# Kernel optimization log

Hardware: AMD Instinct MI355X
Metric: run time of the kernel (lower is better)

Reference implementation:

```python
import jax, jax.numpy as jnp
import numpy as np
import math

B, L, H, E = 4, 1024, 8, 64  # win_size = L
NEG_INF = -1e9  # finite stand-in for -inf causal mask (same softmax result, grad-safe)


def setup_inputs() -> dict:
    key = jax.random.key(0)
    k1, k2, k3, k4 = jax.random.split(key, 4)
    return {
        "queries": jax.random.normal(k1, (B, L, H, E), dtype=jnp.float32),
        "keys": jax.random.normal(k2, (B, L, H, E), dtype=jnp.float32),
        "values": jax.random.normal(k3, (B, L, H, E), dtype=jnp.float32),
        "sigma": jax.random.normal(k4, (B, L, H), dtype=jnp.float32),
    }


def reference(queries, keys, values, sigma):
    b, l, h, e = queries.shape
    scale = 1.0 / math.sqrt(e)

    # attention scores: [B,H,L,S]
    scores = jnp.einsum('blhe,bshe->bhls', queries, keys)
    causal = jnp.triu(jnp.ones((l, l), dtype=bool), k=1)  # mask_flag=True, attn_mask=None
    scores = jnp.where(causal, NEG_INF, scores)
    attn = scale * scores

    # sigma chain: [B,L,H] -> [B,H,L] -> [B,H,L,L]
    s = jnp.transpose(sigma, (0, 2, 1))
    s = jax.nn.sigmoid(s * 5.0) + 1e-5
    s = jnp.power(3.0, s) - 1.0
    sigma4 = jnp.broadcast_to(s[..., None], (b, h, l, l))

    # gaussian prior over |i-j| distances
    idx = jnp.arange(l)
    dist = jnp.abs(idx[:, None] - idx[None, :]).astype(attn.dtype)  # [L,L]
    prior = jnp.exp(-(dist ** 2) / (2.0 * sigma4 ** 2)) / (math.sqrt(2.0 * math.pi) * sigma4)

    series = jax.nn.softmax(attn, axis=-1)  # dropout is identity at eval
    V = jnp.einsum('bhls,bshd->blhd', series, values)
    return V, series, prior, sigma4
```

## Files before the change

kernel.cpp:

```cpp
#include <hip/hip_runtime.h>
#include <math.h>
#include <stdint.h>


#define BB 4
#define LL 1024
#define HH 8
#define EE 64
#define ROWS 32
#define THREADS 1024
#define CHUNK 128

typedef __attribute__((ext_vector_type(8))) short bf16x8;
typedef __attribute__((ext_vector_type(4))) float f32x4;

static constexpr size_t OFF_V      = 0;
static constexpr size_t OFF_SERIES = (size_t)BB * LL * HH * EE;
static constexpr size_t OFF_PRIOR  = OFF_SERIES + (size_t)BB * HH * LL * LL;
static constexpr size_t OFF_SIGMA4 = OFF_PRIOR + (size_t)BB * HH * LL * LL;

static constexpr int LDS_BYTES = 82048;

__device__ __forceinline__ short f2bf(float f) {
    union { float f; uint32_t u; } v; v.f = f;
    uint32_t r = (v.u + 0x7FFFu + ((v.u >> 16) & 1u)) >> 16;
    return (short)r;
}
__device__ __forceinline__ float bf2f(short s) {
    union { uint32_t u; float f; } v; v.u = ((uint32_t)(unsigned short)s) << 16;
    return v.f;
}

__global__ __launch_bounds__(THREADS, 4) void anomaly_attn_kernel(
    const float* __restrict__ Q, const float* __restrict__ K,
    const float* __restrict__ V, float* __restrict__ out)
{
    extern __shared__ char lds[];
    short* sSb  = (short*)lds;
    short* Kb   = (short*)(lds + 65536);
    float* red  = (float*)(lds + 65536);
    float* rinv = (float*)(lds + 81920);

    const int tid  = threadIdx.x;
    const int lane = tid & 63;
    const int w    = tid >> 6;
    const int tile = blockIdx.x & 31;
    const int bh   = blockIdx.x >> 5;
    const int b    = bh >> 3, h = bh & 7;
    const int r0   = tile * ROWS;
    const int NCH  = (r0 + ROWS + CHUNK - 1) / CHUNK;
    const int NC   = NCH * CHUNK;

    const float* Kbase = K + (size_t)b * (LL * HH * EE) + h * EE;
    const float* Vbase = V + (size_t)b * (LL * HH * EE) + h * EE;

    const int jr2 = tid >> 3;
    const int g8  = tid & 7;

    const int rgQ = w >> 3;
    const int cgQ = w & 7;
    bf16x8 qf0, qf1;
    {
        int qrow = r0 + rgQ * 16 + (lane & 15);
        const float* qp = Q + ((size_t)(b * LL + qrow) * HH + h) * EE + ((lane >> 4) << 3);
        float4 a = *(const float4*)qp;
        float4 c = *(const float4*)(qp + 4);
        qf0[0]=f2bf(a.x); qf0[1]=f2bf(a.y); qf0[2]=f2bf(a.z); qf0[3]=f2bf(a.w);
        qf0[4]=f2bf(c.x); qf0[5]=f2bf(c.y); qf0[6]=f2bf(c.z); qf0[7]=f2bf(c.w);
        float4 a2 = *(const float4*)(qp + 32);
        float4 c2 = *(const float4*)(qp + 36);
        qf1[0]=f2bf(a2.x); qf1[1]=f2bf(a2.y); qf1[2]=f2bf(a2.z); qf1[3]=f2bf(a2.w);
        qf1[4]=f2bf(c2.x); qf1[5]=f2bf(c2.y); qf1[6]=f2bf(c2.z); qf1[7]=f2bf(c2.w);
    }

    float4 kp0 = *(const float4*)&Kbase[(size_t)jr2 * 512 + g8 * 8];
    float4 kp1 = *(const float4*)&Kbase[(size_t)jr2 * 512 + g8 * 8 + 4];

    for (int ck = 0; ck < NCH; ++ck) {
        __syncthreads();
        {
            bf16x8 kv;
            kv[0]=f2bf(kp0.x); kv[1]=f2bf(kp0.y); kv[2]=f2bf(kp0.z); kv[3]=f2bf(kp0.w);
            kv[4]=f2bf(kp1.x); kv[5]=f2bf(kp1.y); kv[6]=f2bf(kp1.z); kv[7]=f2bf(kp1.w);
            *(bf16x8*)&Kb[jr2 * 64 + ((g8 ^ (jr2 & 7)) << 3)] = kv;
        }
        if (ck + 1 < NCH) {
            kp0 = *(const float4*)&Kbase[(size_t)((ck + 1) * CHUNK + jr2) * 512 + g8 * 8];
            kp1 = *(const float4*)&Kbase[(size_t)((ck + 1) * CHUNK + jr2) * 512 + g8 * 8 + 4];
        }
        __syncthreads();

        f32x4 acc = {0.f, 0.f, 0.f, 0.f};
        const int jl = cgQ * 16 + (lane & 15);
        {
            int ge = lane >> 4;
            bf16x8 bf = *(const bf16x8*)&Kb[jl * 64 + ((ge ^ (jl & 7)) << 3)];
            acc = __builtin_amdgcn_mfma_f32_16x16x32_bf16(qf0, bf, acc, 0, 0, 0);
            ge = 4 + (lane >> 4);
            bf16x8 bf2 = *(const bf16x8*)&Kb[jl * 64 + ((ge ^ (jl & 7)) << 3)];
            acc = __builtin_amdgcn_mfma_f32_16x16x32_bf16(qf1, bf2, acc, 0, 0, 0);
        }
        int colg = ck * CHUNK + cgQ * 16 + (lane & 15);
        int gc   = colg >> 3;
        int co   = colg & 7;
#pragma unroll
        for (int q = 0; q < 4; ++q) {
            int rt = rgQ * 16 + ((lane >> 4) << 2) + q;
            float e = (colg <= r0 + rt) ? __expf(acc[q] * 0.125f) : 0.f;
            sSb[rt * 1024 + ((gc ^ (rt & 7)) << 3) + co] = f2bf(e);
        }
    }
    __syncthreads();

    float4 vp0 = *(const float4*)&Vbase[(size_t)jr2 * 512 + g8 * 8];
    float4 vp1 = *(const float4*)&Vbase[(size_t)jr2 * 512 + g8 * 8 + 4];

    {
        int r = tid >> 5, j2 = tid & 31;
        float sum = 0.f;
        for (int g = j2; g < (NC >> 3); g += 32) {
            bf16x8 v = *(const bf16x8*)&sSb[r * 1024 + ((g ^ (r & 7)) << 3)];
            float s0 = bf2f(v[0]) + bf2f(v[1]), s1 = bf2f(v[2]) + bf2f(v[3]);
            float s2 = bf2f(v[4]) + bf2f(v[5]), s3 = bf2f(v[6]) + bf2f(v[7]);
            sum += (s0 + s1) + (s2 + s3);
        }
        sum += __shfl_xor(sum, 1);
        sum += __shfl_xor(sum, 2);
        sum += __shfl_xor(sum, 4);
        sum += __shfl_xor(sum, 8);
        sum += __shfl_xor(sum, 16);
        if (j2 == 0) rinv[r] = 1.0f / sum;
    }
    __syncthreads();

    {
        int gc = tid & 127;
        int rb = tid >> 7;
        size_t base = OFF_SERIES + ((size_t)bh * LL + r0) * LL;
#pragma unroll
        for (int it = 0; it < 4; ++it) {
            int r_ = rb + it * 8;
            float4 o0, o1;
            if (gc * 8 < NC) {
                float ri = rinv[r_];
                bf16x8 v = *(const bf16x8*)&sSb[r_ * 1024 + ((gc ^ (r_ & 7)) << 3)];
                o0 = make_float4(bf2f(v[0]) * ri, bf2f(v[1]) * ri, bf2f(v[2]) * ri, bf2f(v[3]) * ri);
                o1 = make_float4(bf2f(v[4]) * ri, bf2f(v[5]) * ri, bf2f(v[6]) * ri, bf2f(v[7]) * ri);
            } else {
                o0 = make_float4(0.f, 0.f, 0.f, 0.f); o1 = o0;
            }
            *(float4*)(out + base + (size_t)r_ * LL + gc * 8)     = o0;
            *(float4*)(out + base + (size_t)r_ * LL + gc * 8 + 4) = o1;
        }
    }

    const int t   = w & 7;
    const int rgP = t >> 2;
    const int egP = t & 3;
    const int kh  = w >> 3;
    f32x4 pacc = {0.f, 0.f, 0.f, 0.f};

    for (int vc = 0; vc < NCH; ++vc) {
        __syncthreads();
        {
            float vv[8] = {vp0.x, vp0.y, vp0.z, vp0.w, vp1.x, vp1.y, vp1.z, vp1.w};
            int jg = jr2 >> 3, jo = jr2 & 7;
#pragma unroll
            for (int i = 0; i < 8; ++i) {
                int e   = g8 * 8 + i;
                int swz = ((e >> 3) ^ e) & 7;
                Kb[e * 128 + ((jg ^ swz) << 3) + jo] = f2bf(vv[i]);
            }
        }
        if (vc + 1 < NCH) {
            vp0 = *(const float4*)&Vbase[(size_t)((vc + 1) * CHUNK + jr2) * 512 + g8 * 8];
            vp1 = *(const float4*)&Vbase[(size_t)((vc + 1) * CHUNK + jr2) * 512 + g8 * 8 + 4];
        }
        __syncthreads();

#pragma unroll
        for (int s = 0; s < 2; ++s) {
            int jl0 = kh * 64 + s * 32;
            int rt  = rgP * 16 + (lane & 15);
            int gg  = ((vc * CHUNK + jl0) >> 3) + (lane >> 4);
            bf16x8 af = *(const bf16x8*)&sSb[rt * 1024 + ((gg ^ (rt & 7)) << 3)];
            int e   = egP * 16 + (lane & 15);
            int jg  = (jl0 >> 3) + (lane >> 4);
            int swz = ((e >> 3) ^ e) & 7;
            bf16x8 bf = *(const bf16x8*)&Kb[e * 128 + ((jg ^ swz) << 3)];
            pacc = __builtin_amdgcn_mfma_f32_16x16x32_bf16(af, bf, pacc, 0, 0, 0);
        }
    }

    __syncthreads();
    if (w < 8) {
        *(f32x4*)&red[(t * 64 + lane) * 4] = pacc;
    }
    __syncthreads();
    if (w >= 8) {
        f32x4 o = *(const f32x4*)&red[(t * 64 + lane) * 4];
#pragma unroll
        for (int q = 0; q < 4; ++q) {
            int rt = rgP * 16 + ((lane >> 4) << 2) + q;
            float val = (pacc[q] + o[q]) * rinv[rt];
            out[OFF_V + ((size_t)(b * LL + r0 + rt) * HH + h) * EE + egP * 16 + (lane & 15)] = val;
        }
    }
}

__global__ __launch_bounds__(256) void anomaly_prior_kernel(
    const float* __restrict__ sigma, float* __restrict__ out)
{
    int bhrow = blockIdx.x;
    int i  = bhrow & (LL - 1);
    int bh = bhrow >> 10;
    int b  = bh >> 3, h = bh & 7;

    float x  = sigma[((size_t)b * LL + i) * HH + h];
    float sg = 1.0f / (1.0f + __expf(-5.0f * x)) + 1e-5f;
    float s  = __expf(1.0986122886681098f * sg) - 1.0f;
    float inv2s2 = 0.5f / (s * s);
    float coef   = 0.3989422804014327f / s;

    size_t rowbase = (size_t)bhrow * LL;
    int j0 = threadIdx.x * 4;

    float d0 = (float)(i - (j0 + 0));
    float d1 = (float)(i - (j0 + 1));
    float d2 = (float)(i - (j0 + 2));
    float d3 = (float)(i - (j0 + 3));
    float4 p = make_float4(coef * __expf(-d0 * d0 * inv2s2),
                           coef * __expf(-d1 * d1 * inv2s2),
                           coef * __expf(-d2 * d2 * inv2s2),
                           coef * __expf(-d3 * d3 * inv2s2));
    *(float4*)(out + OFF_PRIOR + rowbase + j0)  = p;
    *(float4*)(out + OFF_SIGMA4 + rowbase + j0) = make_float4(s, s, s, s);
}

extern "C" void kernel_launch(void* const* d_in, const int* in_sizes, int n_in,
                              void* d_out, int out_size, void* d_ws, size_t ws_size,
                              hipStream_t stream) {
    const float* Q     = (const float*)d_in[0];
    const float* K     = (const float*)d_in[1];
    const float* V     = (const float*)d_in[2];
    const float* sigma = (const float*)d_in[3];
    float* out = (float*)d_out;

    (void)hipFuncSetAttribute((const void*)anomaly_attn_kernel,
                              hipFuncAttributeMaxDynamicSharedMemorySize, LDS_BYTES);

    anomaly_attn_kernel<<<dim3(BB * HH * (LL / ROWS)), dim3(THREADS), LDS_BYTES, stream>>>(Q, K, V, out);
    anomaly_prior_kernel<<<dim3(BB * HH * LL), dim3(256), 0, stream>>>(sigma, out);
}
```

Before: 477.5 us.

## Shrink V staging to 64-row chunks and split reduction to cut LDS

The P·V loop now stages V in 64-row chunks in a smaller transposed LDS buffer, with one MFMA per wave per chunk, and the cross-wave reduction is done in two halves so the scratch buffer is halved. Together these bring the LDS footprint to 80 KB, and the launch bound is raised to allow more waves per SIMD. The aim is higher occupancy so the memory-bound series and prior writes overlap better. In exchange the V loop runs twice as many iterations, each with two barriers, and the epilogue gains two extra barriers.

```diff
diff --git a/kernel.cpp b/kernel.cpp
--- a/kernel.cpp
+++ b/kernel.cpp
@@ -10,6 +10,7 @@
 #define ROWS 32
 #define THREADS 1024
 #define CHUNK 128
+#define VCHUNK 64
 
 typedef __attribute__((ext_vector_type(8))) short bf16x8;
 typedef __attribute__((ext_vector_type(4))) float f32x4;
@@ -19,7 +20,7 @@
 static constexpr size_t OFF_PRIOR  = OFF_SERIES + (size_t)BB * HH * LL * LL;
 static constexpr size_t OFF_SIGMA4 = OFF_PRIOR + (size_t)BB * HH * LL * LL;
 
-static constexpr int LDS_BYTES = 82048;
+static constexpr int LDS_BYTES = 81920;
 
 __device__ __forceinline__ short f2bf(float f) {
     union { float f; uint32_t u; } v; v.f = f;
@@ -31,15 +32,16 @@
     return v.f;
 }
 
-__global__ __launch_bounds__(THREADS, 4) void anomaly_attn_kernel(
+__global__ __launch_bounds__(THREADS, 8) void anomaly_attn_kernel(
     const float* __restrict__ Q, const float* __restrict__ K,
     const float* __restrict__ V, float* __restrict__ out)
 {
     extern __shared__ char lds[];
     short* sSb  = (short*)lds;
     short* Kb   = (short*)(lds + 65536);
-    float* red  = (float*)(lds + 65536);
-    float* rinv = (float*)(lds + 81920);
+    short* Vt   = (short*)(lds + 65536);
+    float* red  = (float*)(lds + 73728);
+    float* rinv = (float*)(lds + 77824);
 
     const int tid  = threadIdx.x;
     const int lane = tid & 63;
@@ -112,8 +114,9 @@
     }
     __syncthreads();
 
-    float4 vp0 = *(const float4*)&Vbase[(size_t)jr2 * 512 + g8 * 8];
-    float4 vp1 = *(const float4*)&Vbase[(size_t)jr2 * 512 + g8 * 8 + 4];
+    const int vj = tid >> 4;
+    const int ve = (tid & 15) * 4;
+    float4 vp = *(const float4*)&Vbase[(size_t)vj * 512 + ve];
 
     {
         int r = tid >> 5, j2 = tid & 31;
@@ -158,52 +161,58 @@
     const int rgP = t >> 2;
     const int egP = t & 3;
     const int kh  = w >> 3;
+    const int NVC = NC / VCHUNK;
     f32x4 pacc = {0.f, 0.f, 0.f, 0.f};
 
-    for (int vc = 0; vc < NCH; ++vc) {
-        __syncthreads();
-        {
-            float vv[8] = {vp0.x, vp0.y, vp0.z, vp0.w, vp1.x, vp1.y, vp1.z, vp1.w};
-            int jg = jr2 >> 3, jo = jr2 & 7;
-#pragma unroll
-            for (int i = 0; i < 8; ++i) {
-                int e   = g8 * 8 + i;
-                int swz = ((e >> 3) ^ e) & 7;
-                Kb[e * 128 + ((jg ^ swz) << 3) + jo] = f2bf(vv[i]);
+    for (int vc = 0; vc < NVC; ++vc) {
+        __syncthreads();
+        {
+            float vv[4] = {vp.x, vp.y, vp.z, vp.w};
+            int jg = vj >> 3, jo = vj & 7;
+#pragma unroll
+            for (int i = 0; i < 4; ++i) {
+                int e = ve + i;
+                Vt[e * 64 + ((jg ^ (e & 7)) << 3) + jo] = f2bf(vv[i]);
             }
         }
-        if (vc + 1 < NCH) {
-            vp0 = *(const float4*)&Vbase[(size_t)((vc + 1) * CHUNK + jr2) * 512 + g8 * 8];
-            vp1 = *(const float4*)&Vbase[(size_t)((vc + 1) * CHUNK + jr2) * 512 + g8 * 8 + 4];
-        }
-        __syncthreads();
-
-#pragma unroll
-        for (int s = 0; s < 2; ++s) {
-            int jl0 = kh * 64 + s * 32;
-            int rt  = rgP * 16 + (lane & 15);
-            int gg  = ((vc * CHUNK + jl0) >> 3) + (lane >> 4);
+        if (vc + 1 < NVC) {
+            vp = *(const float4*)&Vbase[(size_t)((vc + 1) * VCHUNK + vj) * 512 + ve];
+        }
+        __syncthreads();
+
+        {
+            int rt = rgP * 16 + (lane & 15);
+            int gg = vc * 8 + kh * 4 + (lane >> 4);
             bf16x8 af = *(const bf16x8*)&sSb[rt * 1024 + ((gg ^ (rt & 7)) << 3)];
-            int e   = egP * 16 + (lane & 15);
-            int jg  = (jl0 >> 3) + (lane >> 4);
-            int swz = ((e >> 3) ^ e) & 7;
-            bf16x8 bf = *(const bf16x8*)&Kb[e * 128 + ((jg ^ swz) << 3)];
+            int e  = egP * 16 + (lane & 15);
+            int g  = kh * 4 + (lane >> 4);
+            bf16x8 bf = *(const bf16x8*)&Vt[e * 64 + ((g ^ (e & 7)) << 3)];
             pacc = __builtin_amdgcn_mfma_f32_16x16x32_bf16(af, bf, pacc, 0, 0, 0);
         }
     }
 
     __syncthreads();
-    if (w < 8) {
-        *(f32x4*)&red[(t * 64 + lane) * 4] = pacc;
-    }
-    __syncthreads();
-    if (w >= 8) {
+    if (kh == 0 && t < 4) *(f32x4*)&red[(t * 64 + lane) * 4] = pacc;
+    __syncthreads();
+    if (kh == 1 && t < 4) {
         f32x4 o = *(const f32x4*)&red[(t * 64 + lane) * 4];
 #pragma unroll
         for (int q = 0; q < 4; ++q) {
             int rt = rgP * 16 + ((lane >> 4) << 2) + q;
-            float val = (pacc[q] + o[q]) * rinv[rt];
-            out[OFF_V + ((size_t)(b * LL + r0 + rt) * HH + h) * EE + egP * 16 + (lane & 15)] = val;
+            out[OFF_V + ((size_t)(b * LL + r0 + rt) * HH + h) * EE + egP * 16 + (lane & 15)]
+                = (pacc[q] + o[q]) * rinv[rt];
+        }
+    }
+    __syncthreads();
+    if (kh == 0 && t >= 4) *(f32x4*)&red[((t - 4) * 64 + lane) * 4] = pacc;
+    __syncthreads();
+    if (kh == 1 && t >= 4) {
+        f32x4 o = *(const f32x4*)&red[((t - 4) * 64 + lane) * 4];
+#pragma unroll
+        for (int q = 0; q < 4; ++q) {
+            int rt = rgP * 16 + ((lane >> 4) << 2) + q;
+            out[OFF_V + ((size_t)(b * LL + r0 + rt) * HH + h) * EE + egP * 16 + (lane & 15)]
+                = (pacc[q] + o[q]) * rinv[rt];
         }
     }
 }
```

New measurement: 474.0 us. About the same (-0.7%).
